# Performance work log

Measured on AMD Instinct MI355X. Metric: run time of the kernel, lower is better.

The kernel has to match this reference:

```python
import jax, jax.numpy as jnp
import numpy as np

B, T, V, H = 4, 512, 8000, 7


def setup_inputs() -> dict:
    key = jax.random.key(0)
    k1, k2, k3 = jax.random.split(key, 3)
    return {
        "input_ids": jax.random.randint(k1, (B, T), 0, V),
        "frequencies": jax.random.normal(k2, (V,), dtype=jnp.float32) * 3.0,
        "amplitudes": 1.0 + jax.random.normal(k3, (V,), dtype=jnp.float32) * 0.1,
        "decay": jnp.asarray(1.5, dtype=jnp.float32),
        "chunk_size": 16,
    }


def reference(input_ids, frequencies, amplitudes, decay, chunk_size):
    h = jnp.arange(1, H + 1, dtype=frequencies.dtype)  # (H,)
    # harmonic expansion: freqs = f*[1..H], amps = A/[1..H]^decay
    all_f = frequencies[:, None] * h                    # (V, H)
    all_A = amplitudes[:, None] / h ** decay            # (V, H)
    seq_f = frequencies[input_ids][..., None] * h       # (B, T, H)
    seq_A = amplitudes[input_ids][..., None] / h ** decay

    nc = T // chunk_size
    sfc = seq_f.reshape(B, nc, chunk_size, H).transpose(1, 0, 2, 3)  # (nc,B,c,H)
    sAc = seq_A.reshape(B, nc, chunk_size, H).transpose(1, 0, 2, 3)

    def per_chunk(args):
        sf, sA = args  # (B,c,H)
        df = sf[:, :, :, None, None] - all_f[None, None, None, :, :]   # (B,c,H,V,H)
        amp = sA[:, :, :, None, None] * all_A[None, None, None, :, :]
        return 2.0 * (amp * jnp.sinc(2.0 * df)).sum(axis=(2, 4))       # (B,c,V)

    Cc = jax.lax.map(per_chunk, (sfc, sAc))            # (nc, B, c, V)
    C = Cc.transpose(1, 0, 2, 3).reshape(B, T, V)      # (B, T, V)

    cum = jnp.cumsum(C, axis=1)
    # logits[t] uses history 0..t-1 -> shift right by one, position 0 gets zeros
    logits = jnp.concatenate([jnp.zeros_like(cum[:, :1]), cum[:, :-1]], axis=1)
    return logits
```

## Files before the change

kernel.cpp:

```cpp
#include <hip/hip_runtime.h>
#include <math.h>


typedef float v2f __attribute__((ext_vector_type(2)));

constexpr int cB = 4, cT = 512, cV = 8000, cH = 7;
constexpr int GT = 4;
constexpr int NPLANE = 28;

__device__ __forceinline__ v2f pk_add(v2f a, v2f b) {
    v2f d; asm("v_pk_add_f32 %0, %1, %2" : "=v"(d) : "v"(a), "v"(b)); return d;
}
__device__ __forceinline__ v2f pk_mul(v2f a, v2f b) {
    v2f d; asm("v_pk_mul_f32 %0, %1, %2" : "=v"(d) : "v"(a), "v"(b)); return d;
}
__device__ __forceinline__ v2f pk_fma(v2f a, v2f b, v2f c) {
    v2f d; asm("v_pk_fma_f32 %0, %1, %2, %3" : "=v"(d) : "v"(a), "v"(b), "v"(c));
    return d;
}

__global__ __launch_bounds__(256) void wavelm_tab(
    const float* __restrict__ freq, const float* __restrict__ amp,
    const float* __restrict__ decay_p, float* __restrict__ tab)
{
    const int v = blockIdx.x * 256 + threadIdx.x;
    if (v >= cV) return;
    const float decay = decay_p[0];
    const float f = freq[v], A = amp[v];
    const float p2 = __builtin_amdgcn_exp2f(-decay);
    const float p3 = __builtin_amdgcn_exp2f(-decay * 1.5849625007f);
    const float p5 = __builtin_amdgcn_exp2f(-decay * 2.3219280949f);
    const float p7 = __builtin_amdgcn_exp2f(-decay * 2.8073549221f);
    const float rp[7] = {1.f, p2, p3, p2*p2, p5, p2*p3, p7};
    const float xr = f - rintf(f);
    const float s1 = __builtin_amdgcn_sinf(xr);
    const float c1 = __builtin_amdgcn_cosf(xr);
    float s = s1, c = c1;
#pragma unroll
    for (int k = 0; k < cH; ++k) {
        if (k) { const float sp = s, cp = c;
                 s = fmaf(sp, c1,  cp * s1);
                 c = fmaf(cp, c1, -(sp * s1)); }
        tab[(size_t)k * cV + v]        = s;
        tab[(size_t)(7 + k) * cV + v]  = c;
        tab[(size_t)(14 + k) * cV + v] = A * rp[k];
        tab[(size_t)(21 + k) * cV + v] = f * (float)(k + 1);
    }
}

__global__ __launch_bounds__(256) void wavelm_g(
    const int* __restrict__ ids, const float* __restrict__ tab,
    float* __restrict__ out)
{
    const int bt0 = blockIdx.y * GT;
    const int vh  = blockIdx.x * 256 + threadIdx.x;
    const bool valid = (vh * 2 < cV);
    const int vc = valid ? vh : 0;

    const v2f* tp = (const v2f*)tab;
    v2f nb[cH], sBw[cH], cBw[cH];
#pragma unroll
    for (int j = 0; j < cH; ++j) {
        const v2f s = tp[(size_t)j * (cV/2) + vc];
        const v2f c = tp[(size_t)(7 + j) * (cV/2) + vc];
        const v2f w = tp[(size_t)(14 + j) * (cV/2) + vc];
        const v2f a = tp[(size_t)(21 + j) * (cV/2) + vc];
        const v2f ws = w * 0.15915494309189535f;
        sBw[j] = s * ws;
        cBw[j] = c * ws;
        nb[j].x = -a.x;  nb[j].y = -a.y;
    }

    for (int g = 0; g < GT; ++g) {
        const int bt = bt0 + g;
        const int id = ids[bt];
        float sA[cH], cA[cH], wA[cH], aU[cH];
#pragma unroll
        for (int i = 0; i < cH; ++i) {
            sA[i] = tab[(size_t)i * cV + id];
            cA[i] = tab[(size_t)(7 + i) * cV + id];
            wA[i] = tab[(size_t)(14 + i) * cV + id];
            aU[i] = tab[(size_t)(21 + i) * cV + id];
        }

        float accx = 0.f, accy = 0.f;
        float mn = 3.0e38f, mx = 0.0f;
#pragma unroll
        for (int i = 0; i < cH; ++i) {
            v2f ai;  ai.x = aU[i];  ai.y = aU[i];
            v2f d[cH], p[cH];
#pragma unroll
            for (int j = 0; j < cH; ++j) d[j] = pk_add(ai, nb[j]);
            p[0] = d[0];
#pragma unroll
            for (int j = 1; j < cH; ++j) p[j] = pk_mul(p[j-1], d[j]);
            const float ptot = p[6].x * p[6].y;
            mn = fminf(mn, fminf(fabsf(p[6].x), fabsf(p[6].y)));
            mn = fminf(mn, fabsf(ptot));
            mx = fmaxf(mx, fabsf(ptot));
            const float rt = __builtin_amdgcn_rcpf(ptot);
            v2f r;  r.x = rt * p[6].y;  r.y = rt * p[6].x;
            v2f accS = (v2f)0.f, accC = (v2f)0.f;
#pragma unroll
            for (int j = cH - 1; j >= 1; --j) {
                const v2f inv = pk_mul(r, p[j-1]);
                accS = pk_fma(cBw[j], inv, accS);
                accC = pk_fma(sBw[j], inv, accC);
                r = pk_mul(r, d[j]);
            }
            accS = pk_fma(cBw[0], r, accS);
            accC = pk_fma(sBw[0], r, accC);
            const float tx = fmaf(sA[i], accS.x, -(cA[i] * accC.x));
            const float ty = fmaf(sA[i], accS.y, -(cA[i] * accC.y));
            accx = fmaf(wA[i], tx, accx);
            accy = fmaf(wA[i], ty, accy);
        }

        if (mn < 1e-37f || mx > 1e37f) {
            accx = 0.f;  accy = 0.f;
#pragma unroll
            for (int i = 0; i < cH; ++i) {
                float ax = 0.f, ay = 0.f;
#pragma unroll
                for (int j = 0; j < cH; ++j) {
                    const v2f w = tp[(size_t)(14 + j) * (cV/2) + vc];
                    const float dx = aU[i] + nb[j].x;
                    const float dy = aU[i] + nb[j].y;
                    const float snx = fmaf(sA[i], cBw[j].x, -(cA[i] * sBw[j].x));
                    const float sny = fmaf(sA[i], cBw[j].y, -(cA[i] * sBw[j].y));
                    float qx = snx * __builtin_amdgcn_rcpf(dx);
                    float qy = sny * __builtin_amdgcn_rcpf(dy);
                    qx = (dx == 0.f) ? w.x : qx;
                    qy = (dy == 0.f) ? w.y : qy;
                    ax += qx;  ay += qy;
                }
                accx = fmaf(wA[i], ax, accx);
                accy = fmaf(wA[i], ay, accy);
            }
        }

        if (valid) {
            v2f res;  res.x = 2.f * accx;  res.y = 2.f * accy;
            *(v2f*)(out + (size_t)bt * cV + (size_t)vh * 2) = res;
        }
    }
}

__global__ __launch_bounds__(256) void wavelm_seg(
    const float* __restrict__ out, float* __restrict__ segsum,
    int lgseg, int seglen)
{
    const int v = blockIdx.x * 256 + threadIdx.x;
    if (v >= cV) return;
    const int bs = blockIdx.y;
    const int b = bs >> lgseg, seg = bs & ((1 << lgseg) - 1);
    const float* p = out + ((size_t)b * cT + (size_t)seg * seglen) * cV + v;
    float a0 = 0.f, a1 = 0.f, a2 = 0.f, a3 = 0.f;
    for (int k = 0; k < seglen; k += 4) {
        a0 += p[(size_t)(k+0) * cV];
        a1 += p[(size_t)(k+1) * cV];
        a2 += p[(size_t)(k+2) * cV];
        a3 += p[(size_t)(k+3) * cV];
    }
    segsum[(size_t)bs * cV + v] = (a0 + a1) + (a2 + a3);
}

__global__ __launch_bounds__(256) void wavelm_scan2(
    float* __restrict__ out, const float* __restrict__ segsum,
    int lgseg, int seglen)
{
    const int v = blockIdx.x * 256 + threadIdx.x;
    if (v >= cV) return;
    const int bs = blockIdx.y;
    const int b = bs >> lgseg, seg = bs & ((1 << lgseg) - 1);
    const int nseg = 1 << lgseg;
    float base = 0.f;
    for (int sp = 0; sp < seg; ++sp)
        base += segsum[(size_t)(b * nseg + sp) * cV + v];
    float* p = out + ((size_t)b * cT + (size_t)seg * seglen) * cV + v;
    float acc = base;
#pragma unroll 8
    for (int k = 0; k < seglen; ++k) {
        const float c = p[(size_t)k * cV];
        p[(size_t)k * cV] = acc;
        acc += c;
    }
}

__global__ __launch_bounds__(256) void wavelm_scan(float* __restrict__ out)
{
    const int g = blockIdx.x * blockDim.x + threadIdx.x;
    if (g >= cB * cV) return;
    const int b = g / cV;
    const int v = g - b * cV;
    float* p = out + (size_t)b * cT * cV + v;
    float acc = 0.f;
#pragma unroll 8
    for (int t = 0; t < cT; ++t) {
        const float c = p[(size_t)t * cV];
        p[(size_t)t * cV] = acc;
        acc += c;
    }
}

extern "C" void kernel_launch(void* const* d_in, const int* in_sizes, int n_in,
                              void* d_out, int out_size, void* d_ws, size_t ws_size,
                              hipStream_t stream)
{
    const int*   ids  = (const int*)d_in[0];
    const float* freq = (const float*)d_in[1];
    const float* amp  = (const float*)d_in[2];
    const float* dec  = (const float*)d_in[3];
    float* out = (float*)d_out;
    float* tab = (float*)d_ws;
    float* segsum = tab + (size_t)NPLANE * cV;

    const size_t tab_b = (size_t)NPLANE * cV * sizeof(float);
    int lgseg = 4;
    while (lgseg > 0 &&
           tab_b + ((size_t)cB << lgseg) * cV * sizeof(float) > ws_size)
        --lgseg;
    const int use_seg =
        (lgseg > 0 &&
         tab_b + ((size_t)cB << lgseg) * cV * sizeof(float) <= ws_size) ? 1 : 0;

    wavelm_tab<<<(cV + 255) / 256, 256, 0, stream>>>(freq, amp, dec, tab);

    dim3 grid((cV / 2 + 255) / 256, cB * cT / GT);
    wavelm_g<<<grid, dim3(256), 0, stream>>>(ids, tab, out);

    if (use_seg) {
        const int nseg = 1 << lgseg;
        const int seglen = cT / nseg;
        dim3 sg((cV + 255) / 256, cB * nseg);
        wavelm_seg<<<sg, dim3(256), 0, stream>>>(out, segsum, lgseg, seglen);
        wavelm_scan2<<<sg, dim3(256), 0, stream>>>(out, segsum, lgseg, seglen);
    } else {
        const int nchains = cB * cV;
        wavelm_scan<<<(nchains + 255) / 256, dim3(256), 0, stream>>>(out);
    }
}
```

Baseline: 224.6 us.

## Fuse segment-local prefix scan into compute kernel and add segment bases afterwards

The compute kernel now handles 16 timesteps per block and writes exclusive within-segment prefix sums plus a per-segment total, in place of raw contributions. A small kernel scans the segment totals into bases, and a vectorised pass adds each base to its segment. This removes the separate segment-sum read pass and the scalar rescan of the output, and it prefetches the next token's table entries. In exchange there are 4x fewer compute blocks, so occupancy drops, and the output is still read and written once more.

```diff
diff --git a/kernel.cpp b/kernel.cpp
--- a/kernel.cpp
+++ b/kernel.cpp
@@ -3,9 +3,11 @@
 
 
 typedef float v2f __attribute__((ext_vector_type(2)));
+typedef float v4f __attribute__((ext_vector_type(4)));
 
 constexpr int cB = 4, cT = 512, cV = 8000, cH = 7;
-constexpr int GT = 4;
+constexpr int GT = 16;
+constexpr int NSEG = cT / GT;
 constexpr int NPLANE = 28;
 
 __device__ __forceinline__ v2f pk_add(v2f a, v2f b) {
@@ -50,9 +52,10 @@
 
 __global__ __launch_bounds__(256) void wavelm_g(
     const int* __restrict__ ids, const float* __restrict__ tab,
-    float* __restrict__ out)
-{
-    const int bt0 = blockIdx.y * GT;
+    float* __restrict__ out, float* __restrict__ segsum, const int segmode)
+{
+    const int bs  = blockIdx.y;
+    const int bt0 = bs * GT;
     const int vh  = blockIdx.x * 256 + threadIdx.x;
     const bool valid = (vh * 2 < cV);
     const int vc = valid ? vh : 0;
@@ -71,16 +74,30 @@
         nb[j].x = -a.x;  nb[j].y = -a.y;
     }
 
+    float sA[cH], cA[cH], wA[cH], aU[cH];
+    {
+        const int id0 = ids[bt0];
+#pragma unroll
+        for (int i = 0; i < cH; ++i) {
+            sA[i] = tab[(size_t)i * cV + id0];
+            cA[i] = tab[(size_t)(7 + i) * cV + id0];
+            wA[i] = tab[(size_t)(14 + i) * cV + id0];
+            aU[i] = tab[(size_t)(21 + i) * cV + id0];
+        }
+    }
+
+    v2f acc;  acc.x = 0.f;  acc.y = 0.f;
+
     for (int g = 0; g < GT; ++g) {
-        const int bt = bt0 + g;
-        const int id = ids[bt];
-        float sA[cH], cA[cH], wA[cH], aU[cH];
-#pragma unroll
-        for (int i = 0; i < cH; ++i) {
-            sA[i] = tab[(size_t)i * cV + id];
-            cA[i] = tab[(size_t)(7 + i) * cV + id];
-            wA[i] = tab[(size_t)(14 + i) * cV + id];
-            aU[i] = tab[(size_t)(21 + i) * cV + id];
+        const int gn  = (g + 1 < GT) ? g + 1 : g;
+        const int idn = ids[bt0 + gn];
+        float sN[cH], cN[cH], wN[cH], aN[cH];
+#pragma unroll
+        for (int i = 0; i < cH; ++i) {
+            sN[i] = tab[(size_t)i * cV + idn];
+            cN[i] = tab[(size_t)(7 + i) * cV + idn];
+            wN[i] = tab[(size_t)(14 + i) * cV + idn];
+            aN[i] = tab[(size_t)(21 + i) * cV + idn];
         }
 
         float accx = 0.f, accy = 0.f;
@@ -141,49 +158,58 @@
 
         if (valid) {
             v2f res;  res.x = 2.f * accx;  res.y = 2.f * accy;
-            *(v2f*)(out + (size_t)bt * cV + (size_t)vh * 2) = res;
-        }
-    }
-}
-
-__global__ __launch_bounds__(256) void wavelm_seg(
-    const float* __restrict__ out, float* __restrict__ segsum,
-    int lgseg, int seglen)
-{
-    const int v = blockIdx.x * 256 + threadIdx.x;
-    if (v >= cV) return;
-    const int bs = blockIdx.y;
-    const int b = bs >> lgseg, seg = bs & ((1 << lgseg) - 1);
-    const float* p = out + ((size_t)b * cT + (size_t)seg * seglen) * cV + v;
-    float a0 = 0.f, a1 = 0.f, a2 = 0.f, a3 = 0.f;
-    for (int k = 0; k < seglen; k += 4) {
-        a0 += p[(size_t)(k+0) * cV];
-        a1 += p[(size_t)(k+1) * cV];
-        a2 += p[(size_t)(k+2) * cV];
-        a3 += p[(size_t)(k+3) * cV];
-    }
-    segsum[(size_t)bs * cV + v] = (a0 + a1) + (a2 + a3);
-}
-
-__global__ __launch_bounds__(256) void wavelm_scan2(
-    float* __restrict__ out, const float* __restrict__ segsum,
-    int lgseg, int seglen)
-{
-    const int v = blockIdx.x * 256 + threadIdx.x;
-    if (v >= cV) return;
-    const int bs = blockIdx.y;
-    const int b = bs >> lgseg, seg = bs & ((1 << lgseg) - 1);
-    const int nseg = 1 << lgseg;
-    float base = 0.f;
-    for (int sp = 0; sp < seg; ++sp)
-        base += segsum[(size_t)(b * nseg + sp) * cV + v];
-    float* p = out + ((size_t)b * cT + (size_t)seg * seglen) * cV + v;
-    float acc = base;
-#pragma unroll 8
-    for (int k = 0; k < seglen; ++k) {
-        const float c = p[(size_t)k * cV];
-        p[(size_t)k * cV] = acc;
-        acc += c;
+            const size_t o = (size_t)(bt0 + g) * cV + (size_t)vh * 2;
+            v2f wv;  wv.x = segmode ? acc.x : res.x;
+                     wv.y = segmode ? acc.y : res.y;
+            *(v2f*)(out + o) = wv;
+            acc = pk_add(acc, res);
+        }
+
+#pragma unroll
+        for (int i = 0; i < cH; ++i) {
+            sA[i] = sN[i];  cA[i] = cN[i];  wA[i] = wN[i];  aU[i] = aN[i];
+        }
+    }
+
+    if (valid && segmode)
+        *(v2f*)(segsum + (size_t)bs * cV + (size_t)vh * 2) = acc;
+}
+
+__global__ __launch_bounds__(256) void wavelm_bases(float* __restrict__ segsum)
+{
+    const int g = blockIdx.x * 256 + threadIdx.x;
+    if (g >= cB * cV) return;
+    const int b = g / cV;
+    const int v = g - b * cV;
+    float* p = segsum + (size_t)b * NSEG * cV + v;
+    float acc = 0.f;
+#pragma unroll
+    for (int s = 0; s < NSEG; ++s) {
+        const float t = p[(size_t)s * cV];
+        p[(size_t)s * cV] = acc;
+        acc += t;
+    }
+}
+
+__global__ __launch_bounds__(256) void wavelm_addbase(
+    float* __restrict__ out, const float* __restrict__ bases)
+{
+    const int btq = blockIdx.y;
+    const int b  = btq >> 6;
+    const int t0 = (btq & 63) * 8;
+    const int seg = t0 / GT;
+    if (seg == 0) return;
+    const int v4 = blockIdx.x * 256 + threadIdx.x;
+    if (v4 >= cV / 4) return;
+
+    const v4f base = *(const v4f*)(bases +
+        ((size_t)(b * NSEG + seg)) * cV + (size_t)v4 * 4);
+    float* p = out + ((size_t)b * cT + t0) * cV + (size_t)v4 * 4;
+#pragma unroll
+    for (int k = 0; k < 8; ++k) {
+        v4f x = *(v4f*)(p + (size_t)k * cV);
+        x.x += base.x;  x.y += base.y;  x.z += base.z;  x.w += base.w;
+        *(v4f*)(p + (size_t)k * cV) = x;
     }
 }
 
@@ -216,25 +242,19 @@
     float* segsum = tab + (size_t)NPLANE * cV;
 
     const size_t tab_b = (size_t)NPLANE * cV * sizeof(float);
-    int lgseg = 4;
-    while (lgseg > 0 &&
-           tab_b + ((size_t)cB << lgseg) * cV * sizeof(float) > ws_size)
-        --lgseg;
-    const int use_seg =
-        (lgseg > 0 &&
-         tab_b + ((size_t)cB << lgseg) * cV * sizeof(float) <= ws_size) ? 1 : 0;
+    const size_t seg_b = (size_t)cB * NSEG * cV * sizeof(float);
+    const int segmode = (tab_b + seg_b <= ws_size) ? 1 : 0;
 
     wavelm_tab<<<(cV + 255) / 256, 256, 0, stream>>>(freq, amp, dec, tab);
 
     dim3 grid((cV / 2 + 255) / 256, cB * cT / GT);
-    wavelm_g<<<grid, dim3(256), 0, stream>>>(ids, tab, out);
-
-    if (use_seg) {
-        const int nseg = 1 << lgseg;
-        const int seglen = cT / nseg;
-        dim3 sg((cV + 255) / 256, cB * nseg);
-        wavelm_seg<<<sg, dim3(256), 0, stream>>>(out, segsum, lgseg, seglen);
-        wavelm_scan2<<<sg, dim3(256), 0, stream>>>(out, segsum, lgseg, seglen);
+    wavelm_g<<<grid, dim3(256), 0, stream>>>(ids, tab, out, segsum, segmode);
+
+    if (segmode) {
+        const int nchains = cB * cV;
+        wavelm_bases<<<(nchains + 255) / 256, dim3(256), 0, stream>>>(segsum);
+        dim3 ab((cV / 4 + 255) / 256, cB * (cT / 8));
+        wavelm_addbase<<<ab, dim3(256), 0, stream>>>(out, segsum);
     } else {
         const int nchains = cB * cV;
         wavelm_scan<<<(nchains + 255) / 256, dim3(256), 0, stream>>>(out);
```

Result: slower. 232.9 us (+3.7%).
